# Optimization experiments

Measured on AMD Instinct MI355X. Metric: run time of the kernel, lower is better.

The kernel has to match this reference:

```python
import jax, jax.numpy as jnp
import numpy as np

N = 50000   # nodes
E = 800000  # edges
R = 8       # relations
B = 4       # bases
NEG = 0.2   # leaky relu slope


def setup_inputs() -> dict:
    key = jax.random.key(0)
    ks = jax.random.split(key, 20)
    s = 0.1
    rn = lambda k, sh: jax.random.normal(k, sh, dtype=jnp.float32) * s
    return {
        "x": jax.random.normal(ks[0], (N, 64), dtype=jnp.float32),
        "edge_index": jax.random.randint(ks[1], (2, E), 0, N),
        "edge_type": jax.random.randint(ks[2], (E,), 0, R),
        # RGCN layer 1 (64 -> 64), basis decomposition
        "basis1": rn(ks[3], (B, 64, 64)), "comp1": rn(ks[4], (R, B)),
        "root1": rn(ks[5], (64, 64)), "brg1": jnp.zeros((64,), jnp.float32),
        # GAT layer 1 (64 -> 32, heads=4, concat -> 128)
        "wg1": rn(ks[6], (64, 128)), "asrc1": rn(ks[7], (4, 32)),
        "adst1": rn(ks[8], (4, 32)), "bg1": jnp.zeros((128,), jnp.float32),
        # RGCN layer 2 (128 -> 32)
        "basis2": rn(ks[9], (B, 128, 32)), "comp2": rn(ks[10], (R, B)),
        "root2": rn(ks[11], (128, 32)), "brg2": jnp.zeros((32,), jnp.float32),
        # GAT layer 2 (32 -> 16, heads=4, concat=False -> mean)
        "wg2": rn(ks[12], (32, 64)), "asrc2": rn(ks[13], (4, 16)),
        "adst2": rn(ks[14], (4, 16)), "bg2": jnp.zeros((16,), jnp.float32),
    }


def rgcn(x, src, dst, etype, basis, comp, root, bias):
    """PyG RGCNConv with basis decomposition, aggr='mean' per relation."""
    n, f = x.shape
    weight = jnp.einsum('rb,bio->rio', comp, basis)          # [R, in, out]
    seg = dst * R + etype                                    # per (node, relation) segment
    msg = x[src]                                             # [E, in] gather
    sums = jax.ops.segment_sum(msg, seg, num_segments=n * R).reshape(n, R, f)
    cnt = jax.ops.segment_sum(jnp.ones((src.shape[0],), x.dtype), seg,
                              num_segments=n * R).reshape(n, R, 1)
    mean = sums / jnp.maximum(cnt, 1.0)                      # [N, R, in]
    return jnp.einsum('nri,rio->no', mean, weight) + x @ root + bias


def gat(x, src, dst, w, a_src, a_dst, bias, heads, out_ch, concat):
    """PyG GATConv: add self loops, edge softmax over incoming edges."""
    n = x.shape[0]
    loop = jnp.arange(n)
    s2 = jnp.concatenate([src, loop])
    d2 = jnp.concatenate([dst, loop])
    h = (x @ w).reshape(n, heads, out_ch)                    # [N, H, C]
    al_src = (h * a_src).sum(-1)                             # [N, H]
    al_dst = (h * a_dst).sum(-1)                             # [N, H]
    e = jax.nn.leaky_relu(al_src[s2] + al_dst[d2], NEG)      # [E2, H]
    m = jax.ops.segment_max(e, d2, num_segments=n)           # stable softmax per dst
    e = jnp.exp(e - m[d2])
    z = jax.ops.segment_sum(e, d2, num_segments=n)
    alpha = e / z[d2]                                        # [E2, H]
    msg = h[s2] * alpha[:, :, None]                          # [E2, H, C]
    out = jax.ops.segment_sum(msg, d2, num_segments=n)       # [N, H, C]
    out = out.reshape(n, heads * out_ch) if concat else out.mean(axis=1)
    return out + bias


def reference(x, edge_index, edge_type,
              basis1, comp1, root1, brg1, wg1, asrc1, adst1, bg1,
              basis2, comp2, root2, brg2, wg2, asrc2, adst2, bg2):
    src, dst = edge_index[0], edge_index[1]
    # i=0: RGCN + relu (dropout p=0)
    x = jax.nn.relu(rgcn(x, src, dst, edge_type, basis1, comp1, root1, brg1))
    # i=1 == 2*pairs-1: GAT concat, NO activation
    x = gat(x, src, dst, wg1, asrc1, adst1, bg1, heads=4, out_ch=32, concat=True)
    # i=2: RGCN + relu
    x = jax.nn.relu(rgcn(x, src, dst, edge_type, basis2, comp2, root2, brg2))
    # i=3: GAT mean-heads + relu
    x = jax.nn.relu(gat(x, src, dst, wg2, asrc2, adst2, bg2, heads=4, out_ch=16, concat=False))
    return jnp.tanh(x)
```

## Files before the change

kernel.cpp:

```cpp
#include <hip/hip_runtime.h>
#include <math.h>

#define NN 50000
#define EE 800000
#define RR 8
#define SLOPE 0.2f
#define SEGS (NN * RR)
#define NBLK ((SEGS + 255) / 256)
#define NTW ((NN + 63) / 64)
#define NBUK 98
#define SEGB 4096
#define EB4 ((EE + 4095) / 4096)

typedef __attribute__((ext_vector_type(8))) short bf16x8;
typedef __attribute__((ext_vector_type(4))) float f32x4;
typedef _Float16 f16;
typedef __attribute__((ext_vector_type(4))) _Float16 h4;
typedef __attribute__((ext_vector_type(8))) _Float16 h8;

__device__ __forceinline__ float leaky(float v) { return v >= 0.f ? v : SLOPE * v; }

__device__ __forceinline__ void fmacc(float4& a, const float4& v, float p) {
    a.x = fmaf(v.x, p, a.x);
    a.y = fmaf(v.y, p, a.y);
    a.z = fmaf(v.z, p, a.z);
    a.w = fmaf(v.w, p, a.w);
}

__device__ __forceinline__ void red4(float4& a, int m) {
    a.x += __shfl_xor(a.x, m);
    a.y += __shfl_xor(a.y, m);
    a.z += __shfl_xor(a.z, m);
    a.w += __shfl_xor(a.w, m);
}

__device__ __forceinline__ float4 h4tof4(h4 t) {
    return make_float4((float)t.x, (float)t.y, (float)t.z, (float)t.w);
}

__device__ __forceinline__ void split8(const float4& v0, const float4& v1,
                                       bf16x8& hi, bf16x8& lo) {
    float e[8] = {v0.x, v0.y, v0.z, v0.w, v1.x, v1.y, v1.z, v1.w};
    union { bf16x8 v; unsigned u[4]; } H, L;
#pragma unroll
    for (int j = 0; j < 4; j++) {
        unsigned b0 = __float_as_uint(e[2 * j]), b1 = __float_as_uint(e[2 * j + 1]);
        unsigned h0 = b0 & 0xFFFF0000u, h1 = b1 & 0xFFFF0000u;
        H.u[j] = (h0 >> 16) | h1;
        float l0 = e[2 * j] - __uint_as_float(h0);
        float l1 = e[2 * j + 1] - __uint_as_float(h1);
        L.u[j] = (__float_as_uint(l0) >> 16) | (__float_as_uint(l1) & 0xFFFF0000u);
    }
    hi = H.v;
    lo = L.v;
}

__global__ void k_count2(const int* __restrict__ dst, const int* __restrict__ et,
                         int* __restrict__ cnt2) {
    int e = blockIdx.x * 256 + threadIdx.x;
    if (e < EE) atomicAdd(&cnt2[dst[e] * RR + et[e]], 1);
}

__global__ void k_scanA(const int* __restrict__ cnt2, int* __restrict__ rp,
                        int* __restrict__ bsum) {
    __shared__ int sh[256];
    int t = threadIdx.x;
    int i = blockIdx.x * 256 + t;
    int v = (i < SEGS) ? cnt2[i] : 0;
    sh[t] = v;
    __syncthreads();
    for (int off = 1; off < 256; off <<= 1) {
        int u = (t >= off) ? sh[t - off] : 0;
        __syncthreads();
        sh[t] += u;
        __syncthreads();
    }
    if (i < SEGS) rp[i] = sh[t] - v;
    if (t == 255) bsum[blockIdx.x] = sh[255];
}

__global__ void k_scanB(int* __restrict__ bsum) {
    __shared__ int sh[256];
    int t = threadIdx.x;
    int loc[8];
    int s = 0;
#pragma unroll
    for (int i = 0; i < 8; i++) {
        int idx = t * 8 + i;
        int v = (idx < NBLK) ? bsum[idx] : 0;
        loc[i] = v;
        s += v;
    }
    sh[t] = s;
    __syncthreads();
    for (int off = 1; off < 256; off <<= 1) {
        int u = (t >= off) ? sh[t - off] : 0;
        __syncthreads();
        sh[t] += u;
        __syncthreads();
    }
    int run = sh[t] - s;
#pragma unroll
    for (int i = 0; i < 8; i++) {
        int idx = t * 8 + i;
        if (idx < NBLK) {
            int v = loc[i];
            bsum[idx] = run;
            run += v;
        }
    }
}

__global__ void k_scanC(int* __restrict__ rp, const int* __restrict__ bsum) {
    int i = blockIdx.x * 256 + threadIdx.x;
    if (i < SEGS) rp[i] += bsum[blockIdx.x];
    if (i == 0) rp[SEGS] = EE;
}

__global__ void k_initcb(const int* __restrict__ rp, int* __restrict__ cbcur) {
    int t = threadIdx.x;
    if (t < NBUK) cbcur[t] = rp[t * SEGB];
}

__global__ __launch_bounds__(256) void k_fillA(const int* __restrict__ src,
                                               const int* __restrict__ dst,
                                               const int* __restrict__ et,
                                               int* __restrict__ cbcur,
                                               int* __restrict__ recbuf) {
    __shared__ int hist[NBUK], lcur[NBUK], gres[NBUK];
    int tid = threadIdx.x;
    int e0 = blockIdx.x * 4096;
    int cnt = EE - e0;
    if (cnt > 4096) cnt = 4096;
    for (int i = tid; i < NBUK; i += 256) { hist[i] = 0; lcur[i] = 0; }
    __syncthreads();
    int myb[16], myrec[16];
#pragma unroll
    for (int j = 0; j < 16; j++) {
        int i = tid + j * 256;
        if (i < cnt) {
            int e = e0 + i;
            int d = dst[e];
            int b = d >> 9;
            myb[j] = b;
            myrec[j] = ((d & 511) << 19) | (src[e] << 3) | et[e];
            atomicAdd(&hist[b], 1);
        } else {
            myb[j] = -1;
            myrec[j] = 0;
        }
    }
    __syncthreads();
    if (tid < NBUK) gres[tid] = atomicAdd(&cbcur[tid], hist[tid]);
    __syncthreads();
#pragma unroll
    for (int j = 0; j < 16; j++) {
        if (myb[j] >= 0) {
            int p = atomicAdd(&lcur[myb[j]], 1);
            recbuf[gres[myb[j]] + p] = myrec[j];
        }
    }
}

__global__ __launch_bounds__(256) void k_fillB(const int* __restrict__ rp,
                                               const int* __restrict__ recbuf,
                                               int* __restrict__ srcs2) {
    __shared__ int cur[SEGB];
    int b = blockIdx.x;
    int segbase = b * SEGB;
    int nseg = SEGS - segbase;
    if (nseg > SEGB) nseg = SEGB;
    int base = rp[segbase];
    int tid = threadIdx.x;
    for (int s = tid; s < SEGB; s += 256)
        cur[s] = (s < nseg) ? (rp[segbase + s] - base) : 0;
    __syncthreads();
    int limit = rp[segbase + nseg];
    int cnt = limit - base;
    for (int i = tid; i < cnt; i += 256) {
        int rec = recbuf[base + i];
        int segl = ((rec >> 19) << 3) | (rec & 7);
        int p = atomicAdd(&cur[segl], 1);
        srcs2[base + p] = rec & 0x7FFFF;
    }
}

__global__ void k_xh(const float* __restrict__ X, f16* __restrict__ xh) {
    int i = blockIdx.x * 256 + threadIdx.x;
    if (i >= NN * 8) return;
    float4 v0 = *(const float4*)(X + (size_t)i * 8);
    float4 v1 = *(const float4*)(X + (size_t)i * 8 + 4);
    h8 hv = {(f16)v0.x, (f16)v0.y, (f16)v0.z, (f16)v0.w,
             (f16)v1.x, (f16)v1.y, (f16)v1.z, (f16)v1.w};
    *(h8*)(xh + (size_t)i * 8) = hv;
}

__global__ void k_prep(const float* __restrict__ wg1, const float* __restrict__ wg2,
                       const float* __restrict__ root1, const float* __restrict__ root2,
                       const float* __restrict__ basis1, const float* __restrict__ basis2,
                       const float* __restrict__ comp2,
                       const float* __restrict__ asrc1, const float* __restrict__ adst1,
                       const float* __restrict__ asrc2, const float* __restrict__ adst2,
                       float* __restrict__ Wcat2e, float* __restrict__ wg1r,
                       float* __restrict__ Wstk, float* __restrict__ U1p,
                       float* __restrict__ U2p, float* __restrict__ Wb1) {
    int idx = blockIdx.x * 256 + threadIdx.x;
    if (idx < 16384) {
        int h = idx >> 12, kc = idx & 4095;
        int k = kc >> 6, c = kc & 63;
        wg1r[idx] = (c < 32) ? wg1[k * 128 + h * 32 + c] : 0.f;
    } else if (idx < 24576) {
        int j = idx - 16384;
        int row = j >> 6, c = j & 63;
        int h = row >> 5, k = row & 31;
        Wstk[j] = (c < 16) ? wg2[k * 64 + h * 16 + c] : 0.f;
    } else if (idx < 32768) {
        int j = idx - 24576;
        int k = j >> 6, c = j & 63;
        Wcat2e[k * 320 + c] = (c < 32) ? root2[k * 32 + c] : 0.f;
    } else if (idx < 36864) {
        int j0 = idx - 32768;
        int k = j0 >> 6, j = j0 & 63;
        float s = 0.f;
        if (j < 8) {
            int h = j & 3;
            const float* a = (j < 4) ? asrc1 : adst1;
            for (int c = 0; c < 32; c++) s += wg1[k * 128 + h * 32 + c] * a[h * 32 + c];
        }
        U1p[j0] = s;
    } else if (idx < 38912) {
        int j0 = idx - 36864;
        int k = j0 >> 6, j = j0 & 63;
        float s = 0.f;
        if (j < 8) {
            int h = j & 3;
            const float* a = (j < 4) ? asrc2 : adst2;
            for (int c = 0; c < 16; c++) s += wg2[k * 64 + h * 16 + c] * a[h * 16 + c];
        }
        U2p[j0] = s;
    } else if (idx < 55296) {
        Wb1[idx - 38912] = basis1[idx - 38912];
    } else if (idx < 59392) {
        Wb1[idx - 38912] = root1[idx - 55296];
    } else if (idx < 92160) {
        int j = idx - 59392;
        int i = j >> 8, rc = j & 255;
        int r = rc >> 5, o = rc & 31;
        float acc = 0.f;
#pragma unroll
        for (int b = 0; b < 4; b++) acc += comp2[r * 4 + b] * basis2[b * 4096 + i * 32 + o];
        Wcat2e[i * 320 + 64 + rc] = acc;
    }
}

__global__ void k_pack(const float* __restrict__ Wb1, const float* __restrict__ wg1r,
                       const float* __restrict__ Wcat, short* __restrict__ pWb1,
                       short* __restrict__ pwg1r, short* __restrict__ pWcat) {
    int u = blockIdx.x * 256 + threadIdx.x;
    int lane = u & 63, pair = u >> 6;
    if (pair >= 136) return;
    int m = lane & 15, g = lane >> 4;
    const float* src;
    int ldB, col, k0;
    short* dst;
    if (pair < 40) {
        int ct = pair / 10, kc = pair % 10;
        src = Wb1; ldB = 64; col = ct * 16 + m; k0 = kc * 32 + g * 8;
        dst = pWb1 + pair * 1024 + lane * 8;
    } else if (pair < 56) {
        int q = pair - 40;
        int h = q >> 2, lp = q & 3, ct = lp >> 1, kc = lp & 1;
        src = wg1r + h * 4096; ldB = 64; col = ct * 16 + m; k0 = kc * 32 + g * 8;
        dst = pwg1r + q * 1024 + lane * 8;
    } else {
        int q = pair - 56;
        int p = q >> 4, lp = q & 15, ct = lp >> 2, kc = lp & 3;
        src = Wcat; ldB = 320; col = p * 64 + ct * 16 + m; k0 = kc * 32 + g * 8;
        dst = pWcat + q * 1024 + lane * 8;
    }
    float e[8];
#pragma unroll
    for (int r = 0; r < 8; r++) e[r] = src[(size_t)(k0 + r) * ldB + col];
    union { bf16x8 v; unsigned u4[4]; } H, L;
#pragma unroll
    for (int j = 0; j < 4; j++) {
        unsigned b0 = __float_as_uint(e[2 * j]), b1 = __float_as_uint(e[2 * j + 1]);
        unsigned h0 = b0 & 0xFFFF0000u, h1 = b1 & 0xFFFF0000u;
        H.u4[j] = (h0 >> 16) | h1;
        float l0 = e[2 * j] - __uint_as_float(h0);
        float l1 = e[2 * j + 1] - __uint_as_float(h1);
        L.u4[j] = (__float_as_uint(l0) >> 16) | (__float_as_uint(l1) & 0xFFFF0000u);
    }
    *(bf16x8*)dst = H.v;
    *(bf16x8*)(dst + 512) = L.v;
}

template <int KTOT, int NCOL, int ACT = 0, int OUTH = 0, int AH = 0>
__global__ __launch_bounds__(256) void k_mfma(const float* __restrict__ X, int ldX, int xmb,
                                              const short* __restrict__ Bpk, int bmb,
                                              float* __restrict__ Y, int ldY, size_t ymb,
                                              const float* __restrict__ bias, int biasmb) {
    constexpr int NKC = KTOT / 32;
    constexpr int NCT = NCOL / 16;
    const int tid = threadIdx.x;
    const int wid = tid >> 6, lane = tid & 63;
    const int m = lane & 15, g = lane >> 4;
    const int mb = blockIdx.y;
    const int rowbase = blockIdx.x * 64 + wid * 16;
    if (rowbase >= NN) return;
    const float* Xm = X + (size_t)mb * xmb + (size_t)(rowbase + m) * ldX;
    const f16* Xmh = (const f16*)X + (size_t)mb * xmb + (size_t)(rowbase + m) * ldX;
    const short* Bm = Bpk + (size_t)mb * bmb;

    f32x4 acc[NCT];
#pragma unroll
    for (int c = 0; c < NCT; c++) acc[c] = (f32x4){0.f, 0.f, 0.f, 0.f};

#pragma unroll
    for (int kc = 0; kc < NKC; kc++) {
        float4 v0, v1;
        if (AH) {
            h8 hv = *(const h8*)(Xmh + kc * 32 + g * 8);
            v0 = make_float4((float)hv[0], (float)hv[1], (float)hv[2], (float)hv[3]);
            v1 = make_float4((float)hv[4], (float)hv[5], (float)hv[6], (float)hv[7]);
        } else {
            v0 = *(const float4*)(Xm + kc * 32 + g * 8);
            v1 = *(const float4*)(Xm + kc * 32 + g * 8 + 4);
        }
        bf16x8 ah, al;
        split8(v0, v1, ah, al);
#pragma unroll
        for (int ct = 0; ct < NCT; ct++) {
            const short* bp = Bm + (size_t)(ct * NKC + kc) * 1024 + lane * 8;
            bf16x8 bh = *(const bf16x8*)bp;
            bf16x8 bl = *(const bf16x8*)(bp + 512);
            acc[ct] = __builtin_amdgcn_mfma_f32_16x16x32_bf16(ah, bh, acc[ct], 0, 0, 0);
            acc[ct] = __builtin_amdgcn_mfma_f32_16x16x32_bf16(al, bh, acc[ct], 0, 0, 0);
            acc[ct] = __builtin_amdgcn_mfma_f32_16x16x32_bf16(ah, bl, acc[ct], 0, 0, 0);
        }
    }

#pragma unroll
    for (int ct = 0; ct < NCT; ct++) {
        int col = ct * 16 + m;
        float bv = bias ? bias[mb * biasmb + col] : 0.f;
#pragma unroll
        for (int i = 0; i < 4; i++) {
            float o = acc[ct][i] + bv;
            if (ACT == 2) o = fmaxf(o, 0.f);
            if (OUTH) {
                f16* Yh = (f16*)Y;
                Yh[(size_t)mb * ymb + (size_t)(rowbase + g * 4 + i) * ldY + col] = (f16)o;
            } else {
                Y[(size_t)mb * ymb + (size_t)(rowbase + g * 4 + i) * ldY + col] = o;
            }
        }
    }
}

__global__ __launch_bounds__(256) void k_gagg1(const int* __restrict__ rp,
                                               const int* __restrict__ srcs2,
                                               const float* __restrict__ comp,
                                               const f16* __restrict__ Xh,
                                               f16* __restrict__ Uh) {
    __shared__ float4 sh_w[4][8];
    int wid = threadIdx.x >> 6, lane = threadIdx.x & 63;
    int n = blockIdx.x * 4 + wid;
    int rpv = (lane <= 8) ? rp[n * RR + lane] : 0;
    int nxt = __shfl(rpv, (lane + 1) & 63);
    if (lane < 8) {
        float inv = 1.f / (float)((nxt - rpv) > 0 ? (nxt - rpv) : 1);
        float4 c = *(const float4*)(comp + lane * 4);
        sh_w[wid][lane] = make_float4(c.x * inv, c.y * inv, c.z * inv, c.w * inv);
    }
    int q = lane & 15;
    int beg = rp[n * RR], end = rp[n * RR + RR];
    float4 a0 = make_float4(0.f, 0.f, 0.f, 0.f);
    float4 a1 = a0, a2 = a0, a3 = a0;
    int k = beg + (lane >> 4);
    for (; k + 4 < end; k += 8) {
        int key0 = srcs2[k], key1 = srcs2[k + 4];
        float4 w0 = sh_w[wid][key0 & 7], w1 = sh_w[wid][key1 & 7];
        float4 v0 = h4tof4(*(const h4*)(Xh + (size_t)(key0 >> 3) * 64 + q * 4));
        float4 v1 = h4tof4(*(const h4*)(Xh + (size_t)(key1 >> 3) * 64 + q * 4));
        fmacc(a0, v0, w0.x);
        fmacc(a1, v0, w0.y);
        fmacc(a2, v0, w0.z);
        fmacc(a3, v0, w0.w);
        fmacc(a0, v1, w1.x);
        fmacc(a1, v1, w1.y);
        fmacc(a2, v1, w1.z);
        fmacc(a3, v1, w1.w);
    }
    if (k < end) {
        int key0 = srcs2[k];
        float4 w0 = sh_w[wid][key0 & 7];
        float4 v0 = h4tof4(*(const h4*)(Xh + (size_t)(key0 >> 3) * 64 + q * 4));
        fmacc(a0, v0, w0.x);
        fmacc(a1, v0, w0.y);
        fmacc(a2, v0, w0.z);
        fmacc(a3, v0, w0.w);
    }
    red4(a0, 16); red4(a0, 32);
    red4(a1, 16); red4(a1, 32);
    red4(a2, 16); red4(a2, 32);
    red4(a3, 16); red4(a3, 32);
    if (lane < 16) {
        f16* un = Uh + (size_t)n * 320;
        h4 o0 = {(f16)a0.x, (f16)a0.y, (f16)a0.z, (f16)a0.w};
        h4 o1 = {(f16)a1.x, (f16)a1.y, (f16)a1.z, (f16)a1.w};
        h4 o2 = {(f16)a2.x, (f16)a2.y, (f16)a2.z, (f16)a2.w};
        h4 o3 = {(f16)a3.x, (f16)a3.y, (f16)a3.z, (f16)a3.w};
        *(h4*)(un + 0 * 64 + q * 4) = o0;
        *(h4*)(un + 1 * 64 + q * 4) = o1;
        *(h4*)(un + 2 * 64 + q * 4) = o2;
        *(h4*)(un + 3 * 64 + q * 4) = o3;
        *(h4*)(un + 256 + q * 4) = *(const h4*)(Xh + (size_t)n * 64 + q * 4);
    }
}

__global__ __launch_bounds__(256) void k_alds1(const float* __restrict__ X,
                                               const float* __restrict__ U1p,
                                               f16* __restrict__ aldsEh,
                                               f16* __restrict__ x1h) {
    __shared__ float sUT[8 * 68];
    int tid = threadIdx.x;
    for (int i = tid; i < 512; i += 256) {
        int j = i >> 6, c = i & 63;
        sUT[j * 68 + c] = U1p[c * 64 + j];
    }
    __syncthreads();
    int lane = tid & 63, wid = tid >> 6;
    int n = blockIdx.x * 32 + wid * 8 + (lane >> 3);
    int q = lane & 7;
    float x[8];
    if (n < NN) {
        float4 v0 = *(const float4*)(X + (size_t)n * 64 + q * 8);
        float4 v1 = *(const float4*)(X + (size_t)n * 64 + q * 8 + 4);
        x[0] = v0.x; x[1] = v0.y; x[2] = v0.z; x[3] = v0.w;
        x[4] = v1.x; x[5] = v1.y; x[6] = v1.z; x[7] = v1.w;
        h8 hv;
#pragma unroll
        for (int c = 0; c < 8; c++) hv[c] = (f16)x[c];
        *(h8*)(x1h + (size_t)n * 64 + q * 8) = hv;
    } else {
#pragma unroll
        for (int c = 0; c < 8; c++) x[c] = 0.f;
    }
    float al[8];
#pragma unroll
    for (int j = 0; j < 8; j++) {
        const float* u = &sUT[j * 68 + q * 8];
        float s = 0.f;
#pragma unroll
        for (int c = 0; c < 8; c++) s += x[c] * u[c];
        al[j] = s;
    }
#pragma unroll
    for (int m = 1; m < 8; m <<= 1)
#pragma unroll
        for (int j = 0; j < 8; j++) al[j] += __shfl_xor(al[j], m);
    if (n < NN) {
        float av = al[q];
        int pos = (q < 4) ? q : q + 4;
        aldsEh[(size_t)n * 16 + pos] = (f16)__expf(av);
        aldsEh[(size_t)n * 16 + pos + 4] = (f16)__expf(SLOPE * av);
    }
}

__global__ __launch_bounds__(256) void k_final(const f16* __restrict__ Xm,
                                               const float* __restrict__ Wstk,
                                               const float* __restrict__ bg2,
                                               float* __restrict__ out) {
    __shared__ float sWT[16 * 132];
    int tid = threadIdx.x;
    for (int i = tid; i < 2048; i += 256) {
        int c = i >> 7, k = i & 127;
        sWT[c * 132 + k] = Wstk[k * 64 + c];
    }
    __syncthreads();
    int lane = tid & 63, wid = tid >> 6;
    int n = blockIdx.x * 32 + wid * 8 + (lane >> 3);
    int q = lane & 7;
    float x[16];
    if (n < NN) {
#pragma unroll
        for (int t = 0; t < 4; t++) {
            float4 v = h4tof4(*(const h4*)(Xm + (size_t)n * 128 + t * 32 + q * 4));
            x[t * 4 + 0] = v.x; x[t * 4 + 1] = v.y; x[t * 4 + 2] = v.z; x[t * 4 + 3] = v.w;
        }
    } else {
#pragma unroll
        for (int k = 0; k < 16; k++) x[k] = 0.f;
    }
    float al[16];
#pragma unroll
    for (int c = 0; c < 16; c++) {
        float s = 0.f;
#pragma unroll
        for (int t = 0; t < 4; t++) {
            const float* w = &sWT[c * 132 + t * 32 + q * 4];
            s += x[t * 4 + 0] * w[0] + x[t * 4 + 1] * w[1] + x[t * 4 + 2] * w[2] +
                 x[t * 4 + 3] * w[3];
        }
        al[c] = s;
    }
#pragma unroll
    for (int m = 1; m < 8; m <<= 1)
#pragma unroll
        for (int c = 0; c < 16; c++) al[c] += __shfl_xor(al[c], m);
    if (n < NN && q < 4) {
        float4 bv = *(const float4*)(bg2 + q * 4);
        float4 v;
        v.x = tanhf(fmaxf(0.25f * al[q * 4 + 0] + bv.x, 0.f));
        v.y = tanhf(fmaxf(0.25f * al[q * 4 + 1] + bv.y, 0.f));
        v.z = tanhf(fmaxf(0.25f * al[q * 4 + 2] + bv.z, 0.f));
        v.w = tanhf(fmaxf(0.25f * al[q * 4 + 3] + bv.w, 0.f));
        *(float4*)(out + (size_t)n * 16 + q * 4) = v;
    }
}

__global__ __launch_bounds__(256) void k_agg2(const int* __restrict__ rp,
                                              const int* __restrict__ srcs2,
                                              const f16* __restrict__ y,
                                              const float* __restrict__ bias,
                                              const float* __restrict__ U2p,
                                              const float* __restrict__ x3prev,
                                              f16* __restrict__ x3h,
                                              f16* __restrict__ aldsEh) {
    __shared__ float sh_inv[4][8];
    int wid = threadIdx.x >> 6, lane = threadIdx.x & 63;
    int n = blockIdx.x * 4 + wid;
    int rpv = (lane <= 8) ? rp[n * RR + lane] : 0;
    int nxt = __shfl(rpv, (lane + 1) & 63);
    if (lane < 8) sh_inv[wid][lane] = 1.f / (float)((nxt - rpv) > 0 ? (nxt - rpv) : 1);
    int q = lane & 7;
    int beg = rp[n * RR], end = rp[n * RR + RR];
    float4 acc = make_float4(0.f, 0.f, 0.f, 0.f);
    int k = beg + (lane >> 3);
    for (; k + 8 < end; k += 16) {
        int key0 = srcs2[k], key1 = srcs2[k + 8];
        int s0 = key0 >> 3, s1 = key1 >> 3;
        int g0 = key0 & 7, g1 = key1 & 7;
        float e0 = sh_inv[wid][g0], e1 = sh_inv[wid][g1];
        float4 v0 = h4tof4(*(const h4*)(y + ((size_t)(g0 >> 1) * NN + s0) * 64 + (g0 & 1) * 32 + q * 4));
        float4 v1 = h4tof4(*(const h4*)(y + ((size_t)(g1 >> 1) * NN + s1) * 64 + (g1 & 1) * 32 + q * 4));
        fmacc(acc, v0, e0);
        fmacc(acc, v1, e1);
    }
    if (k < end) {
        int key0 = srcs2[k];
        int s0 = key0 >> 3;
        int g0 = key0 & 7;
        float4 v0 = h4tof4(*(const h4*)(y + ((size_t)(g0 >> 1) * NN + s0) * 64 + (g0 & 1) * 32 + q * 4));
        fmacc(acc, v0, sh_inv[wid][g0]);
    }
    red4(acc, 8);
    red4(acc, 16);
    red4(acc, 32);
    if (lane < 8) {
        float4 prev = *(const float4*)(x3prev + (size_t)n * 64 + q * 4);
        float4 b = *(const float4*)(bias + q * 4);
        float4 v;
        v.x = fmaxf(prev.x + acc.x + b.x, 0.f);
        v.y = fmaxf(prev.y + acc.y + b.y, 0.f);
        v.z = fmaxf(prev.z + acc.z + b.z, 0.f);
        v.w = fmaxf(prev.w + acc.w + b.w, 0.f);
        h4 hv = {(f16)v.x, (f16)v.y, (f16)v.z, (f16)v.w};
        *(h4*)(x3h + (size_t)n * 32 + q * 4) = hv;
        float al[8];
#pragma unroll
        for (int j = 0; j < 8; j++) {
            al[j] = fmaf(v.x, U2p[(q * 4 + 0) * 64 + j],
                    fmaf(v.y, U2p[(q * 4 + 1) * 64 + j],
                    fmaf(v.z, U2p[(q * 4 + 2) * 64 + j],
                         v.w * U2p[(q * 4 + 3) * 64 + j])));
        }
#pragma unroll
        for (int m = 1; m < 8; m <<= 1) {
#pragma unroll
            for (int j = 0; j < 8; j++) al[j] += __shfl_xor(al[j], m);
        }
        float av = al[q];
        int pos = (q < 4) ? q : q + 4;
        aldsEh[(size_t)n * 16 + pos] = (f16)__expf(av);
        aldsEh[(size_t)n * 16 + pos + 4] = (f16)__expf(SLOPE * av);
    }
}

template <int F, int LDX = F>
__global__ __launch_bounds__(256) void k_gatx(const int* __restrict__ rp,
                                              const int* __restrict__ srcs2,
                                              const f16* __restrict__ aldsEh,
                                              const f16* __restrict__ X,
                                              f16* __restrict__ msg) {
    constexpr int G = F / 4;
    constexpr int NG = 64 / G;
    int wid = threadIdx.x >> 6, lane = threadIdx.x & 63;
    int n = blockIdx.x * 4 + wid;
    if (n >= NN) return;
    int g = lane / G, q = lane % G;
    h8 ed8 = *(const h8*)(aldsEh + (size_t)n * 16 + 8);
    float4 Ed = make_float4((float)ed8[0], (float)ed8[1], (float)ed8[2], (float)ed8[3]);
    float4 Ed2 = make_float4((float)ed8[4], (float)ed8[5], (float)ed8[6], (float)ed8[7]);
    float4 acc0 = make_float4(0.f, 0.f, 0.f, 0.f);
    float4 acc1 = acc0, acc2 = acc0, acc3 = acc0;
    float4 z = make_float4(0.f, 0.f, 0.f, 0.f);
    if (g == 0) {
        h8 es8 = *(const h8*)(aldsEh + (size_t)n * 16);
        float4 xv = h4tof4(*(const h4*)(X + (size_t)n * LDX + q * 4));
        float p0 = fmaxf((float)es8[0] * Ed.x, (float)es8[4] * Ed2.x);
        float p1 = fmaxf((float)es8[1] * Ed.y, (float)es8[5] * Ed2.y);
        float p2 = fmaxf((float)es8[2] * Ed.z, (float)es8[6] * Ed2.z);
        float p3 = fmaxf((float)es8[3] * Ed.w, (float)es8[7] * Ed2.w);
        z = make_float4(p0, p1, p2, p3);
        fmacc(acc0, xv, p0);
        fmacc(acc1, xv, p1);
        fmacc(acc2, xv, p2);
        fmacc(acc3, xv, p3);
    }
    int beg = rp[n * RR], end = rp[n * RR + RR];
    int k = beg + g;
    for (; k + NG < end; k += 2 * NG) {
        int s0 = srcs2[k] >> 3, s1 = srcs2[k + NG] >> 3;
        h8 e0 = *(const h8*)(aldsEh + (size_t)s0 * 16);
        h8 e1 = *(const h8*)(aldsEh + (size_t)s1 * 16);
        float4 x0 = h4tof4(*(const h4*)(X + (size_t)s0 * LDX + q * 4));
        float4 x1v = h4tof4(*(const h4*)(X + (size_t)s1 * LDX + q * 4));
        float p00 = fmaxf((float)e0[0] * Ed.x, (float)e0[4] * Ed2.x);
        float p01 = fmaxf((float)e0[1] * Ed.y, (float)e0[5] * Ed2.y);
        float p02 = fmaxf((float)e0[2] * Ed.z, (float)e0[6] * Ed2.z);
        float p03 = fmaxf((float)e0[3] * Ed.w, (float)e0[7] * Ed2.w);
        float p10 = fmaxf((float)e1[0] * Ed.x, (float)e1[4] * Ed2.x);
        float p11 = fmaxf((float)e1[1] * Ed.y, (float)e1[5] * Ed2.y);
        float p12 = fmaxf((float)e1[2] * Ed.z, (float)e1[6] * Ed2.z);
        float p13 = fmaxf((float)e1[3] * Ed.w, (float)e1[7] * Ed2.w);
        z.x += p00 + p10;
        z.y += p01 + p11;
        z.z += p02 + p12;
        z.w += p03 + p13;
        fmacc(acc0, x0, p00);
        fmacc(acc1, x0, p01);
        fmacc(acc2, x0, p02);
        fmacc(acc3, x0, p03);
        fmacc(acc0, x1v, p10);
        fmacc(acc1, x1v, p11);
        fmacc(acc2, x1v, p12);
        fmacc(acc3, x1v, p13);
    }
    if (k < end) {
        int s0 = srcs2[k] >> 3;
        h8 e0 = *(const h8*)(aldsEh + (size_t)s0 * 16);
        float4 x0 = h4tof4(*(const h4*)(X + (size_t)s0 * LDX + q * 4));
        float p00 = fmaxf((float)e0[0] * Ed.x, (float)e0[4] * Ed2.x);
        float p01 = fmaxf((float)e0[1] * Ed.y, (float)e0[5] * Ed2.y);
        float p02 = fmaxf((float)e0[2] * Ed.z, (float)e0[6] * Ed2.z);
        float p03 = fmaxf((float)e0[3] * Ed.w, (float)e0[7] * Ed2.w);
        z.x += p00;
        z.y += p01;
        z.z += p02;
        z.w += p03;
        fmacc(acc0, x0, p00);
        fmacc(acc1, x0, p01);
        fmacc(acc2, x0, p02);
        fmacc(acc3, x0, p03);
    }
#pragma unroll
    for (int m = G; m < 64; m <<= 1) {
        red4(acc0, m);
        red4(acc1, m);
        red4(acc2, m);
        red4(acc3, m);
        red4(z, m);
    }
    if (g == 0) {
        float4 iz = make_float4(1.f / z.x, 1.f / z.y, 1.f / z.z, 1.f / z.w);
        f16* mp = msg + (size_t)n * 4 * F + q * 4;
        h4 o0 = {(f16)(acc0.x * iz.x), (f16)(acc0.y * iz.x), (f16)(acc0.z * iz.x), (f16)(acc0.w * iz.x)};
        h4 o1 = {(f16)(acc1.x * iz.y), (f16)(acc1.y * iz.y), (f16)(acc1.z * iz.y), (f16)(acc1.w * iz.y)};
        h4 o2 = {(f16)(acc2.x * iz.z), (f16)(acc2.y * iz.z), (f16)(acc2.z * iz.z), (f16)(acc2.w * iz.z)};
        h4 o3 = {(f16)(acc3.x * iz.w), (f16)(acc3.y * iz.w), (f16)(acc3.z * iz.w), (f16)(acc3.w * iz.w)};
        *(h4*)(mp + 0 * F) = o0;
        *(h4*)(mp + 1 * F) = o1;
        *(h4*)(mp + 2 * F) = o2;
        *(h4*)(mp + 3 * F) = o3;
    }
}

extern "C" void kernel_launch(void* const* d_in, const int* in_sizes, int n_in,
                              void* d_out, int out_size, void* d_ws, size_t ws_size,
                              hipStream_t stream) {
    const float* x      = (const float*)d_in[0];
    const int*   ei     = (const int*)d_in[1];
    const int*   et     = (const int*)d_in[2];
    const float* basis1 = (const float*)d_in[3];
    const float* comp1  = (const float*)d_in[4];
    const float* root1  = (const float*)d_in[5];
    const float* brg1   = (const float*)d_in[6];
    const float* wg1    = (const float*)d_in[7];
    const float* asrc1  = (const float*)d_in[8];
    const float* adst1  = (const float*)d_in[9];
    const float* bg1    = (const float*)d_in[10];
    const float* basis2 = (const float*)d_in[11];
    const float* comp2  = (const float*)d_in[12];
    const float* root2  = (const float*)d_in[13];
    const float* brg2   = (const float*)d_in[14];
    const float* wg2    = (const float*)d_in[15];
    const float* asrc2  = (const float*)d_in[16];
    const float* adst2  = (const float*)d_in[17];
    const float* bg2    = (const float*)d_in[18];
    const int* src = ei;
    const int* dst = ei + EE;
    float* out = (float*)d_out;

    int* wsi = (int*)d_ws;
    size_t ioff = 0;
    auto ialloc = [&](size_t n) { int* p = wsi + ioff; ioff += (n + 3) & ~(size_t)3; return p; };
    int* cnt2 = ialloc(SEGS);
    int* rp   = ialloc(SEGS + 1);
    int* bsum = ialloc(2048);
    int* srcs2 = ialloc(EE);
    int* recbuf = ialloc(EE);
    int* cbcur = ialloc(128);
    float* wsf = (float*)(wsi + ioff);
    size_t total_f = (ws_size - ioff * sizeof(int)) / sizeof(float);
    size_t P_f = (size_t)NN * 320;
    size_t need_f = P_f + (size_t)NN * 128
                  + 40960 + 20480 + 16384 + 8192 + 4096 + 2048
                  + (size_t)NN * 8
                  + 20480 + 8192 + 40960
                  + (size_t)NN * 32 + (size_t)NN * 16 + (size_t)NN * 32 + 64;
    if (total_f < need_f) return;
    size_t foff = 0;
    auto falloc = [&](size_t n) { float* p = wsf + foff; foff += (n + 3) & ~(size_t)3; return p; };
    float* P      = falloc(P_f);
    float* x2     = falloc((size_t)NN * 128);
    float* Wcat2e = falloc(40960);
    float* Wb1    = falloc(20480);
    float* wg1r   = falloc(16384);
    float* Wstk   = falloc(8192);
    float* U1p    = falloc(4096);
    float* U2p    = falloc(2048);
    f16* aldsEh   = (f16*)falloc((size_t)NN * 8);
    short* Wb1pk  = (short*)falloc(20480);
    short* wg1rpk = (short*)falloc(8192);
    short* Wcatpk = (short*)falloc(40960);
    f16* x1h      = (f16*)falloc((size_t)NN * 32);
    f16* x3h      = (f16*)falloc((size_t)NN * 16);
    f16* xh       = (f16*)falloc((size_t)NN * 32);
    f16* Uh = (f16*)P;
    float* x1   = x2 + (size_t)NN * 64;
    f16* msg1h  = (f16*)P;
    float* x3   = P;
    f16* ybuf3h = (f16*)(P + (size_t)NN * 64);
    f16* msg2h  = (f16*)(P + (size_t)NN * 64);

    const int EB = (EE + 255) / 256;
    const int NB4 = (NN + 3) / 4;
    const int NB32 = (NN + 31) / 32;

    hipMemsetAsync(cnt2, 0, SEGS * sizeof(int), stream);
    k_count2<<<EB, 256, 0, stream>>>(dst, et, cnt2);
    k_scanA<<<NBLK, 256, 0, stream>>>(cnt2, rp, bsum);
    k_scanB<<<1, 256, 0, stream>>>(bsum);
    k_scanC<<<NBLK, 256, 0, stream>>>(rp, bsum);
    k_initcb<<<1, 128, 0, stream>>>(rp, cbcur);
    k_fillA<<<EB4, 256, 0, stream>>>(src, dst, et, cbcur, recbuf);
    k_fillB<<<NBUK, 256, 0, stream>>>(rp, recbuf, srcs2);
    k_xh<<<(NN * 8 + 255) / 256, 256, 0, stream>>>(x, xh);
    k_prep<<<(92160 + 255) / 256, 256, 0, stream>>>(
        wg1, wg2, root1, root2, basis1, basis2, comp2, asrc1, adst1, asrc2, adst2,
        Wcat2e, wg1r, Wstk, U1p, U2p, Wb1);
    k_pack<<<34, 256, 0, stream>>>(Wb1, wg1r, Wcat2e, Wb1pk, wg1rpk, Wcatpk);

    k_gagg1<<<NB4, 256, 0, stream>>>(rp, srcs2, comp1, xh, Uh);
    k_mfma<320, 64, 2, 0, 1><<<dim3(NTW, 1), 256, 0, stream>>>((const float*)Uh, 320, 0,
                                                               Wb1pk, 0,
                                                               x1, 64, 0, brg1, 0);

    k_alds1<<<NB32, 256, 0, stream>>>(x1, U1p, aldsEh, x1h);
    k_gatx<64, 64><<<NB4, 256, 0, stream>>>(rp, srcs2, aldsEh, x1h, msg1h);
    k_mfma<64, 32, 0, 0, 1><<<dim3(NTW, 4), 256, 0, stream>>>((const float*)msg1h, 256, 64,
                                                              wg1rpk, 4096,
                                                              x2, 128, 32, bg1, 32);

    k_mfma<128, 64, 0, 0><<<dim3(NTW, 1), 256, 0, stream>>>(x2, 128, 0, Wcatpk, 0,
                                                            P, 64, 0, nullptr, 0);
    k_mfma<128, 64, 0, 1><<<dim3(NTW, 4), 256, 0, stream>>>(x2, 128, 0, Wcatpk + 16384, 16384,
                                                            (float*)ybuf3h, 64, (size_t)NN * 64,
                                                            nullptr, 0);
    k_agg2<<<NB4, 256, 0, stream>>>(rp, srcs2, ybuf3h, brg2, U2p, x3, x3h, aldsEh);

    k_gatx<32, 32><<<NB4, 256, 0, stream>>>(rp, srcs2, aldsEh, x3h, msg2h);
    k_final<<<NB32, 256, 0, stream>>>(msg2h, Wstk, bg2, out);
}
```

Measured before the change: 435.5 us.

## Build CSR via coarse bucket histogram and per-bucket local scan; fp16 attention products

Replaces the global per-segment count, three-pass scan and cb init with a shared-memory bucket histogram over 98 coarse buckets, a tiny scan, and a fillB kernel that counts and scans segments locally per bucket while writing row pointers. This removes the 400K-entry memset, the global atomic counting pass and the multi-kernel scan. The GAT aggregation kernel also computes the exp-product and max in packed fp16 instead of fp32, which cuts conversion instructions at some cost in precision.

```diff
diff --git a/kernel.cpp b/kernel.cpp
--- a/kernel.cpp
+++ b/kernel.cpp
@@ -6,7 +6,6 @@
 #define RR 8
 #define SLOPE 0.2f
 #define SEGS (NN * RR)
-#define NBLK ((SEGS + 255) / 256)
 #define NTW ((NN + 63) / 64)
 #define NBUK 98
 #define SEGB 4096
@@ -35,7 +34,16 @@
 }
 
 __device__ __forceinline__ float4 h4tof4(h4 t) {
-    return make_float4((float)t.x, (float)t.y, (float)t.z, (float)t.w);
+    return make_float4((float)t[0], (float)t[1], (float)t[2], (float)t[3]);
+}
+
+__device__ __forceinline__ h4 hmax4(h4 a, h4 b) {
+    h4 r;
+    r[0] = a[0] > b[0] ? a[0] : b[0];
+    r[1] = a[1] > b[1] ? a[1] : b[1];
+    r[2] = a[2] > b[2] ? a[2] : b[2];
+    r[3] = a[3] > b[3] ? a[3] : b[3];
+    return r;
 }
 
 __device__ __forceinline__ void split8(const float4& v0, const float4& v1,
@@ -55,71 +63,37 @@
     lo = L.v;
 }
 
-__global__ void k_count2(const int* __restrict__ dst, const int* __restrict__ et,
-                         int* __restrict__ cnt2) {
-    int e = blockIdx.x * 256 + threadIdx.x;
-    if (e < EE) atomicAdd(&cnt2[dst[e] * RR + et[e]], 1);
-}
-
-__global__ void k_scanA(const int* __restrict__ cnt2, int* __restrict__ rp,
-                        int* __restrict__ bsum) {
-    __shared__ int sh[256];
+__global__ __launch_bounds__(256) void k_hist(const int* __restrict__ dst,
+                                              int* __restrict__ buccnt) {
+    __shared__ int h[NBUK];
+    int tid = threadIdx.x;
+    for (int i = tid; i < NBUK; i += 256) h[i] = 0;
+    __syncthreads();
+    int e0 = blockIdx.x * 4096;
+    int cnt = EE - e0;
+    if (cnt > 4096) cnt = 4096;
+    for (int i = tid; i < cnt; i += 256) atomicAdd(&h[dst[e0 + i] >> 9], 1);
+    __syncthreads();
+    for (int i = tid; i < NBUK; i += 256)
+        if (h[i]) atomicAdd(&buccnt[i], h[i]);
+}
+
+__global__ void k_scan98(const int* __restrict__ buccnt, int* __restrict__ bucbase,
+                         int* __restrict__ cbcur) {
+    __shared__ int sh[128];
     int t = threadIdx.x;
-    int i = blockIdx.x * 256 + t;
-    int v = (i < SEGS) ? cnt2[i] : 0;
+    int v = (t < NBUK) ? buccnt[t] : 0;
     sh[t] = v;
     __syncthreads();
-    for (int off = 1; off < 256; off <<= 1) {
+    for (int off = 1; off < 128; off <<= 1) {
         int u = (t >= off) ? sh[t - off] : 0;
         __syncthreads();
         sh[t] += u;
         __syncthreads();
     }
-    if (i < SEGS) rp[i] = sh[t] - v;
-    if (t == 255) bsum[blockIdx.x] = sh[255];
-}
-
-__global__ void k_scanB(int* __restrict__ bsum) {
-    __shared__ int sh[256];
-    int t = threadIdx.x;
-    int loc[8];
-    int s = 0;
-#pragma unroll
-    for (int i = 0; i < 8; i++) {
-        int idx = t * 8 + i;
-        int v = (idx < NBLK) ? bsum[idx] : 0;
-        loc[i] = v;
-        s += v;
-    }
-    sh[t] = s;
-    __syncthreads();
-    for (int off = 1; off < 256; off <<= 1) {
-        int u = (t >= off) ? sh[t - off] : 0;
-        __syncthreads();
-        sh[t] += u;
-        __syncthreads();
-    }
-    int run = sh[t] - s;
-#pragma unroll
-    for (int i = 0; i < 8; i++) {
-        int idx = t * 8 + i;
-        if (idx < NBLK) {
-            int v = loc[i];
-            bsum[idx] = run;
-            run += v;
-        }
-    }
-}
-
-__global__ void k_scanC(int* __restrict__ rp, const int* __restrict__ bsum) {
-    int i = blockIdx.x * 256 + threadIdx.x;
-    if (i < SEGS) rp[i] += bsum[blockIdx.x];
-    if (i == 0) rp[SEGS] = EE;
-}
-
-__global__ void k_initcb(const int* __restrict__ rp, int* __restrict__ cbcur) {
-    int t = threadIdx.x;
-    if (t < NBUK) cbcur[t] = rp[t * SEGB];
+    int excl = sh[t] - v;
+    if (t <= NBUK) bucbase[t] = excl;
+    if (t < NBUK) cbcur[t] = excl;
 }
 
 __global__ __launch_bounds__(256) void k_fillA(const int* __restrict__ src,
@@ -162,27 +136,57 @@
     }
 }
 
-__global__ __launch_bounds__(256) void k_fillB(const int* __restrict__ rp,
-                                               const int* __restrict__ recbuf,
-                                               int* __restrict__ srcs2) {
-    __shared__ int cur[SEGB];
+__global__ __launch_bounds__(256) void k_fillB2(const int* __restrict__ bucbase,
+                                                const int* __restrict__ recbuf,
+                                                int* __restrict__ rp,
+                                                int* __restrict__ srcs2) {
+    __shared__ int cnt[SEGB];
+    __shared__ int psc[256];
     int b = blockIdx.x;
     int segbase = b * SEGB;
     int nseg = SEGS - segbase;
     if (nseg > SEGB) nseg = SEGB;
-    int base = rp[segbase];
+    int base = bucbase[b];
+    int cntE = bucbase[b + 1] - base;
     int tid = threadIdx.x;
-    for (int s = tid; s < SEGB; s += 256)
-        cur[s] = (s < nseg) ? (rp[segbase + s] - base) : 0;
-    __syncthreads();
-    int limit = rp[segbase + nseg];
-    int cnt = limit - base;
-    for (int i = tid; i < cnt; i += 256) {
+    for (int s = tid; s < SEGB; s += 256) cnt[s] = 0;
+    __syncthreads();
+    for (int i = tid; i < cntE; i += 256) {
         int rec = recbuf[base + i];
         int segl = ((rec >> 19) << 3) | (rec & 7);
-        int p = atomicAdd(&cur[segl], 1);
+        atomicAdd(&cnt[segl], 1);
+    }
+    __syncthreads();
+    int loc[16];
+    int sbase = tid * 16;
+    int run = 0;
+#pragma unroll
+    for (int j = 0; j < 16; j++) { loc[j] = cnt[sbase + j]; run += loc[j]; }
+    psc[tid] = run;
+    __syncthreads();
+    for (int off = 1; off < 256; off <<= 1) {
+        int u = (tid >= off) ? psc[tid - off] : 0;
+        __syncthreads();
+        psc[tid] += u;
+        __syncthreads();
+    }
+    int excl = psc[tid] - run;
+#pragma unroll
+    for (int j = 0; j < 16; j++) {
+        int s = sbase + j;
+        int v = loc[j];
+        cnt[s] = excl;
+        if (s < nseg) rp[segbase + s] = base + excl;
+        excl += v;
+    }
+    __syncthreads();
+    for (int i = tid; i < cntE; i += 256) {
+        int rec = recbuf[base + i];
+        int segl = ((rec >> 19) << 3) | (rec & 7);
+        int p = atomicAdd(&cnt[segl], 1);
         srcs2[base + p] = rec & 0x7FFFF;
     }
+    if (b == NBUK - 1 && tid == 0) rp[SEGS] = EE;
 }
 
 __global__ void k_xh(const float* __restrict__ X, f16* __restrict__ xh) {
@@ -600,19 +604,17 @@
     int n = blockIdx.x * 4 + wid;
     if (n >= NN) return;
     int g = lane / G, q = lane % G;
-    h8 ed8 = *(const h8*)(aldsEh + (size_t)n * 16 + 8);
-    float4 Ed = make_float4((float)ed8[0], (float)ed8[1], (float)ed8[2], (float)ed8[3]);
-    float4 Ed2 = make_float4((float)ed8[4], (float)ed8[5], (float)ed8[6], (float)ed8[7]);
+    h4 EdH = *(const h4*)(aldsEh + (size_t)n * 16 + 8);
+    h4 Ed2H = *(const h4*)(aldsEh + (size_t)n * 16 + 12);
     float4 acc0 = make_float4(0.f, 0.f, 0.f, 0.f);
     float4 acc1 = acc0, acc2 = acc0, acc3 = acc0;
     float4 z = make_float4(0.f, 0.f, 0.f, 0.f);
     if (g == 0) {
-        h8 es8 = *(const h8*)(aldsEh + (size_t)n * 16);
+        h4 es = *(const h4*)(aldsEh + (size_t)n * 16);
+        h4 es2 = *(const h4*)(aldsEh + (size_t)n * 16 + 4);
         float4 xv = h4tof4(*(const h4*)(X + (size_t)n * LDX + q * 4));
-        float p0 = fmaxf((float)es8[0] * Ed.x, (float)es8[4] * Ed2.x);
-        float p1 = fmaxf((float)es8[1] * Ed.y, (float)es8[5] * Ed2.y);
-        float p2 = fmaxf((float)es8[2] * Ed.z, (float)es8[6] * Ed2.z);
-        float p3 = fmaxf((float)es8[3] * Ed.w, (float)es8[7] * Ed2.w);
+        h4 pH = hmax4(es * EdH, es2 * Ed2H);
+        float p0 = (float)pH[0], p1 = (float)pH[1], p2 = (float)pH[2], p3 = (float)pH[3];
         z = make_float4(p0, p1, p2, p3);
         fmacc(acc0, xv, p0);
         fmacc(acc1, xv, p1);
@@ -627,14 +629,14 @@
         h8 e1 = *(const h8*)(aldsEh + (size_t)s1 * 16);
         float4 x0 = h4tof4(*(const h4*)(X + (size_t)s0 * LDX + q * 4));
         float4 x1v = h4tof4(*(const h4*)(X + (size_t)s1 * LDX + q * 4));
-        float p00 = fmaxf((float)e0[0] * Ed.x, (float)e0[4] * Ed2.x);
-        float p01 = fmaxf((float)e0[1] * Ed.y, (float)e0[5] * Ed2.y);
-        float p02 = fmaxf((float)e0[2] * Ed.z, (float)e0[6] * Ed2.z);
-        float p03 = fmaxf((float)e0[3] * Ed.w, (float)e0[7] * Ed2.w);
-        float p10 = fmaxf((float)e1[0] * Ed.x, (float)e1[4] * Ed2.x);
-        float p11 = fmaxf((float)e1[1] * Ed.y, (float)e1[5] * Ed2.y);
-        float p12 = fmaxf((float)e1[2] * Ed.z, (float)e1[6] * Ed2.z);
-        float p13 = fmaxf((float)e1[3] * Ed.w, (float)e1[7] * Ed2.w);
+        h4 e0lo = {e0[0], e0[1], e0[2], e0[3]};
+        h4 e0hi = {e0[4], e0[5], e0[6], e0[7]};
+        h4 e1lo = {e1[0], e1[1], e1[2], e1[3]};
+        h4 e1hi = {e1[4], e1[5], e1[6], e1[7]};
+        h4 p0H = hmax4(e0lo * EdH, e0hi * Ed2H);
+        h4 p1H = hmax4(e1lo * EdH, e1hi * Ed2H);
+        float p00 = (float)p0H[0], p01 = (float)p0H[1], p02 = (float)p0H[2], p03 = (float)p0H[3];
+        float p10 = (float)p1H[0], p11 = (float)p1H[1], p12 = (float)p1H[2], p13 = (float)p1H[3];
         z.x += p00 + p10;
         z.y += p01 + p11;
         z.z += p02 + p12;
@@ -652,10 +654,10 @@
         int s0 = srcs2[k] >> 3;
         h8 e0 = *(const h8*)(aldsEh + (size_t)s0 * 16);
         float4 x0 = h4tof4(*(const h4*)(X + (size_t)s0 * LDX + q * 4));
-        float p00 = fmaxf((float)e0[0] * Ed.x, (float)e0[4] * Ed2.x);
-        float p01 = fmaxf((float)e0[1] * Ed.y, (float)e0[5] * Ed2.y);
-        float p02 = fmaxf((float)e0[2] * Ed.z, (float)e0[6] * Ed2.z);
-        float p03 = fmaxf((float)e0[3] * Ed.w, (float)e0[7] * Ed2.w);
+        h4 e0lo = {e0[0], e0[1], e0[2], e0[3]};
+        h4 e0hi = {e0[4], e0[5], e0[6], e0[7]};
+        h4 p0H = hmax4(e0lo * EdH, e0hi * Ed2H);
+        float p00 = (float)p0H[0], p01 = (float)p0H[1], p02 = (float)p0H[2], p03 = (float)p0H[3];
         z.x += p00;
         z.y += p01;
         z.z += p02;
@@ -716,12 +718,12 @@
     int* wsi = (int*)d_ws;
     size_t ioff = 0;
     auto ialloc = [&](size_t n) { int* p = wsi + ioff; ioff += (n + 3) & ~(size_t)3; return p; };
-    int* cnt2 = ialloc(SEGS);
     int* rp   = ialloc(SEGS + 1);
-    int* bsum = ialloc(2048);
     int* srcs2 = ialloc(EE);
     int* recbuf = ialloc(EE);
     int* cbcur = ialloc(128);
+    int* buccnt = ialloc(128);
+    int* bucbase = ialloc(128);
     float* wsf = (float*)(wsi + ioff);
     size_t total_f = (ws_size - ioff * sizeof(int)) / sizeof(float);
     size_t P_f = (size_t)NN * 320;
@@ -755,18 +757,14 @@
     f16* ybuf3h = (f16*)(P + (size_t)NN * 64);
     f16* msg2h  = (f16*)(P + (size_t)NN * 64);
 
-    const int EB = (EE + 255) / 256;
     const int NB4 = (NN + 3) / 4;
     const int NB32 = (NN + 31) / 32;
 
-    hipMemsetAsync(cnt2, 0, SEGS * sizeof(int), stream);
-    k_count2<<<EB, 256, 0, stream>>>(dst, et, cnt2);
-    k_scanA<<<NBLK, 256, 0, stream>>>(cnt2, rp, bsum);
-    k_scanB<<<1, 256, 0, stream>>>(bsum);
-    k_scanC<<<NBLK, 256, 0, stream>>>(rp, bsum);
-    k_initcb<<<1, 128, 0, stream>>>(rp, cbcur);
+    hipMemsetAsync(buccnt, 0, 128 * sizeof(int), stream);
+    k_hist<<<EB4, 256, 0, stream>>>(dst, buccnt);
+    k_scan98<<<1, 128, 0, stream>>>(buccnt, bucbase, cbcur);
     k_fillA<<<EB4, 256, 0, stream>>>(src, dst, et, cbcur, recbuf);
-    k_fillB<<<NBUK, 256, 0, stream>>>(rp, recbuf, srcs2);
+    k_fillB2<<<NBUK, 256, 0, stream>>>(bucbase, recbuf, rp, srcs2);
     k_xh<<<(NN * 8 + 255) / 256, 256, 0, stream>>>(x, xh);
     k_prep<<<(92160 + 255) / 256, 256, 0, stream>>>(
         wg1, wg2, root1, root2, basis1, basis2, comp2, asrc1, adst1, asrc2, adst2,
```

New measurement: 403.1 us. 7.4% less time.
